# Kernel optimization log

Measured on AMD Instinct MI355X. Metric: run time of the kernel, lower is better.

The kernel has to match this reference:

```python
import jax, jax.numpy as jnp
import numpy as np


def setup_inputs() -> dict:
    key = jax.random.key(0)
    B, D = 1024, 65536
    inputs = jax.random.normal(key, (B, D), dtype=jnp.float32)
    return {"inputs": inputs, "k": 1024}


def reference(inputs, k):
    # top_k along last axis (matches tf.math.top_k)
    top_k_vals, _ = jax.lax.top_k(inputs, k)          # [B, k]
    # tf.math.reduce_min with no axis -> global scalar threshold
    threshold = jnp.min(top_k_vals)
    mask = jnp.where(inputs >= threshold, jnp.float32(1.0), jnp.float32(0.0))
    return mask * inputs
```

## Files before the change

### kernel.cpp

```cpp
#include <hip/hip_runtime.h>
#include <stdint.h>

#define TPB 256
#define NB1 2048
#define NB2 2048
#define NB3 1024
#define CAP 4096
#define DCOLS 65536

__device__ __forceinline__ unsigned f2key(float f) {
  unsigned u = __float_as_uint(f);
  unsigned m = ((int)u >> 31) | 0x80000000u;
  return u ^ m;
}
__device__ __forceinline__ float key2f(unsigned k) {
  unsigned u = (k & 0x80000000u) ? (k ^ 0x80000000u) : ~k;
  return __uint_as_float(u);
}

__device__ void find_top(const unsigned* hist, int NB, unsigned K,
                         unsigned* scan, unsigned* selbin, unsigned* selrem) {
  const int tid = threadIdx.x;
  const int C = NB / TPB;
  unsigned cs = 0;
  for (int i = 0; i < C; ++i) cs += hist[tid * C + i];
  scan[tid] = cs;
  __syncthreads();
  unsigned suff = cs;
  for (int off = 1; off < TPB; off <<= 1) {
    unsigned add = (tid + off < TPB) ? scan[tid + off] : 0u;
    __syncthreads();
    suff += add;
    scan[tid] = suff;
    __syncthreads();
  }
  unsigned above = suff - cs;
  if (above < K && suff >= K) {
    unsigned cAbove = above;
    for (int bin = tid * C + C - 1; bin >= tid * C; --bin) {
      unsigned c = hist[bin];
      if (cAbove + c >= K) { *selbin = (unsigned)bin; *selrem = K - cAbove; break; }
      cAbove += c;
    }
  }
  __syncthreads();
}

__global__ void __launch_bounds__(TPB)
topk_select(const float* __restrict__ in, const int* __restrict__ kptr,
            unsigned* __restrict__ rowkey) {
  __shared__ unsigned h1[NB1];
  __shared__ unsigned h2[NB2];
  __shared__ unsigned h3[NB3];
  __shared__ unsigned cand[CAP];
  __shared__ unsigned scan[TPB];
  __shared__ unsigned sel_bin, sel_rem, cand_cnt;

  const int tid = threadIdx.x;
  const int row = blockIdx.x;
  const unsigned K = (unsigned)(*kptr);

  for (int i = tid; i < NB1; i += TPB) h1[i] = 0u;
  for (int i = tid; i < NB2; i += TPB) h2[i] = 0u;
  for (int i = tid; i < NB3; i += TPB) h3[i] = 0u;
  if (tid == 0) cand_cnt = 0u;
  __syncthreads();

  const float4* rowv = (const float4*)(in + (size_t)row * DCOLS);
  const int n4 = DCOLS / 4;

  for (int i = tid; i < n4; i += TPB) {
    float4 v = rowv[i];
    atomicAdd(&h1[f2key(v.x) >> 21], 1u);
    atomicAdd(&h1[f2key(v.y) >> 21], 1u);
    atomicAdd(&h1[f2key(v.z) >> 21], 1u);
    atomicAdd(&h1[f2key(v.w) >> 21], 1u);
  }
  __syncthreads();
  find_top(h1, NB1, K, scan, &sel_bin, &sel_rem);
  const unsigned b1 = sel_bin;
  const unsigned K2 = sel_rem;
  __syncthreads();

  for (int i = tid; i < n4; i += TPB) {
    float4 v = rowv[i];
    unsigned kk;
    kk = f2key(v.x);
    if ((kk >> 21) == b1) { atomicAdd(&h2[(kk >> 10) & (NB2 - 1)], 1u);
      unsigned p = atomicAdd(&cand_cnt, 1u); if (p < CAP) cand[p] = kk; }
    kk = f2key(v.y);
    if ((kk >> 21) == b1) { atomicAdd(&h2[(kk >> 10) & (NB2 - 1)], 1u);
      unsigned p = atomicAdd(&cand_cnt, 1u); if (p < CAP) cand[p] = kk; }
    kk = f2key(v.z);
    if ((kk >> 21) == b1) { atomicAdd(&h2[(kk >> 10) & (NB2 - 1)], 1u);
      unsigned p = atomicAdd(&cand_cnt, 1u); if (p < CAP) cand[p] = kk; }
    kk = f2key(v.w);
    if ((kk >> 21) == b1) { atomicAdd(&h2[(kk >> 10) & (NB2 - 1)], 1u);
      unsigned p = atomicAdd(&cand_cnt, 1u); if (p < CAP) cand[p] = kk; }
  }
  __syncthreads();
  find_top(h2, NB2, K2, scan, &sel_bin, &sel_rem);
  const unsigned b2 = sel_bin;
  const unsigned K3 = sel_rem;
  const unsigned nc = cand_cnt;
  __syncthreads();

  if (nc <= CAP) {
    for (unsigned i = tid; i < nc; i += TPB) {
      unsigned kk = cand[i];
      if (((kk >> 10) & (NB2 - 1)) == b2) atomicAdd(&h3[kk & (NB3 - 1)], 1u);
    }
  } else {
    const unsigned pfx = (b1 << 11) | b2;
    for (int i = tid; i < n4; i += TPB) {
      float4 v = rowv[i];
      unsigned kk;
      kk = f2key(v.x); if ((kk >> 10) == pfx) atomicAdd(&h3[kk & (NB3 - 1)], 1u);
      kk = f2key(v.y); if ((kk >> 10) == pfx) atomicAdd(&h3[kk & (NB3 - 1)], 1u);
      kk = f2key(v.z); if ((kk >> 10) == pfx) atomicAdd(&h3[kk & (NB3 - 1)], 1u);
      kk = f2key(v.w); if ((kk >> 10) == pfx) atomicAdd(&h3[kk & (NB3 - 1)], 1u);
    }
  }
  __syncthreads();
  find_top(h3, NB3, K3, scan, &sel_bin, &sel_rem);
  if (tid == 0) rowkey[row] = (b1 << 21) | (b2 << 10) | sel_bin;
}

__global__ void __launch_bounds__(TPB)
minreduce(const unsigned* __restrict__ rowkey, unsigned* __restrict__ thr, int n) {
  __shared__ unsigned s[TPB];
  unsigned m = 0xFFFFFFFFu;
  for (int i = threadIdx.x; i < n; i += TPB) m = min(m, rowkey[i]);
  s[threadIdx.x] = m;
  __syncthreads();
  for (int off = TPB / 2; off > 0; off >>= 1) {
    if (threadIdx.x < off) s[threadIdx.x] = min(s[threadIdx.x], s[threadIdx.x + off]);
    __syncthreads();
  }
  if (threadIdx.x == 0) thr[0] = s[0];
}

__global__ void __launch_bounds__(TPB)
maskk(const float4* __restrict__ in, float4* __restrict__ out,
      const unsigned* __restrict__ thrkey, int n4) {
  const float thr = key2f(thrkey[0]);
  int idx = blockIdx.x * TPB + threadIdx.x;
  int stride = gridDim.x * TPB;
  for (int i = idx; i < n4; i += stride) {
    float4 v = in[i];
    float4 o;
    o.x = (v.x >= thr) ? v.x : 0.0f;
    o.y = (v.y >= thr) ? v.y : 0.0f;
    o.z = (v.z >= thr) ? v.z : 0.0f;
    o.w = (v.w >= thr) ? v.w : 0.0f;
    out[i] = o;
  }
}

extern "C" void kernel_launch(void* const* d_in, const int* in_sizes, int n_in,
                              void* d_out, int out_size, void* d_ws, size_t ws_size,
                              hipStream_t stream) {
  const float* in = (const float*)d_in[0];
  const int* kptr = (const int*)d_in[1];
  float* out = (float*)d_out;
  unsigned* rowkey = (unsigned*)d_ws;
  unsigned* thr = rowkey + 1024;

  const int B = in_sizes[0] / DCOLS;
  const int n4 = out_size / 4;

  hipLaunchKernelGGL(topk_select, dim3(B), dim3(TPB), 0, stream, in, kptr, rowkey);
  hipLaunchKernelGGL(minreduce, dim3(1), dim3(TPB), 0, stream, rowkey, thr, B);
  hipLaunchKernelGGL(maskk, dim3(2048), dim3(TPB), 0, stream,
                     (const float4*)in, (float4*)out, thr, n4);
}
```

Baseline: 538.6 us.

## Use sampled threshold to filter candidates and radix-select in shared memory

Builds a coarse histogram from the first 4096 elements of each row to estimate a conservative threshold near the k/8 sample rank. One full pass then compacts every element above that threshold into shared memory using wave ballot and one atomic per wave. All three radix-select levels run on that candidate list, which replaces two full-row passes with many per-element shared atomics. If the sample gives too few or too many candidates, it falls back to the original three full passes. The mask kernel grid is also doubled.

```diff
diff --git a/kernel.cpp b/kernel.cpp
--- a/kernel.cpp
+++ b/kernel.cpp
@@ -2,11 +2,11 @@
 #include <stdint.h>
 
 #define TPB 256
-#define NB1 2048
-#define NB2 2048
+#define NBH 2048
 #define NB3 1024
-#define CAP 4096
+#define CAP 6144
 #define DCOLS 65536
+#define NSAMP 4096
 
 __device__ __forceinline__ unsigned f2key(float f) {
   unsigned u = __float_as_uint(f);
@@ -16,6 +16,10 @@
 __device__ __forceinline__ float key2f(unsigned k) {
   unsigned u = (k & 0x80000000u) ? (k ^ 0x80000000u) : ~k;
   return __uint_as_float(u);
+}
+
+__device__ __forceinline__ void clear_hist(unsigned* hist, int NB) {
+  for (int i = threadIdx.x; i < NB; i += TPB) hist[i] = 0u;
 }
 
 __device__ void find_top(const unsigned* hist, int NB, unsigned K,
@@ -49,81 +53,129 @@
 __global__ void __launch_bounds__(TPB)
 topk_select(const float* __restrict__ in, const int* __restrict__ kptr,
             unsigned* __restrict__ rowkey) {
-  __shared__ unsigned h1[NB1];
-  __shared__ unsigned h2[NB2];
-  __shared__ unsigned h3[NB3];
+  __shared__ unsigned hist[NBH];
+  __shared__ unsigned scan[TPB];
   __shared__ unsigned cand[CAP];
-  __shared__ unsigned scan[TPB];
   __shared__ unsigned sel_bin, sel_rem, cand_cnt;
 
   const int tid = threadIdx.x;
+  const int lane = tid & 63;
   const int row = blockIdx.x;
   const unsigned K = (unsigned)(*kptr);
-
-  for (int i = tid; i < NB1; i += TPB) h1[i] = 0u;
-  for (int i = tid; i < NB2; i += TPB) h2[i] = 0u;
-  for (int i = tid; i < NB3; i += TPB) h3[i] = 0u;
-  if (tid == 0) cand_cnt = 0u;
-  __syncthreads();
-
   const float4* rowv = (const float4*)(in + (size_t)row * DCOLS);
   const int n4 = DCOLS / 4;
 
+  clear_hist(hist, NBH);
+  if (tid == 0) cand_cnt = 0u;
+  __syncthreads();
+  for (int j = 0; j < NSAMP / 4 / TPB; ++j) {
+    float4 v = rowv[tid + j * TPB];
+    atomicAdd(&hist[f2key(v.x) >> 21], 1u);
+    atomicAdd(&hist[f2key(v.y) >> 21], 1u);
+    atomicAdd(&hist[f2key(v.z) >> 21], 1u);
+    atomicAdd(&hist[f2key(v.w) >> 21], 1u);
+  }
+  __syncthreads();
+  unsigned ksamp = K >> 3;
+  if (ksamp < 32u) ksamp = 32u;
+  if (ksamp > NSAMP - 1) ksamp = NSAMP - 1;
+  find_top(hist, NBH, ksamp, scan, &sel_bin, &sel_rem);
+  const unsigned tlo = sel_bin << 21;
+  __syncthreads();
+
   for (int i = tid; i < n4; i += TPB) {
     float4 v = rowv[i];
-    atomicAdd(&h1[f2key(v.x) >> 21], 1u);
-    atomicAdd(&h1[f2key(v.y) >> 21], 1u);
-    atomicAdd(&h1[f2key(v.z) >> 21], 1u);
-    atomicAdd(&h1[f2key(v.w) >> 21], 1u);
-  }
-  __syncthreads();
-  find_top(h1, NB1, K, scan, &sel_bin, &sel_rem);
-  const unsigned b1 = sel_bin;
-  const unsigned K2 = sel_rem;
-  __syncthreads();
-
-  for (int i = tid; i < n4; i += TPB) {
-    float4 v = rowv[i];
-    unsigned kk;
-    kk = f2key(v.x);
-    if ((kk >> 21) == b1) { atomicAdd(&h2[(kk >> 10) & (NB2 - 1)], 1u);
-      unsigned p = atomicAdd(&cand_cnt, 1u); if (p < CAP) cand[p] = kk; }
-    kk = f2key(v.y);
-    if ((kk >> 21) == b1) { atomicAdd(&h2[(kk >> 10) & (NB2 - 1)], 1u);
-      unsigned p = atomicAdd(&cand_cnt, 1u); if (p < CAP) cand[p] = kk; }
-    kk = f2key(v.z);
-    if ((kk >> 21) == b1) { atomicAdd(&h2[(kk >> 10) & (NB2 - 1)], 1u);
-      unsigned p = atomicAdd(&cand_cnt, 1u); if (p < CAP) cand[p] = kk; }
-    kk = f2key(v.w);
-    if ((kk >> 21) == b1) { atomicAdd(&h2[(kk >> 10) & (NB2 - 1)], 1u);
-      unsigned p = atomicAdd(&cand_cnt, 1u); if (p < CAP) cand[p] = kk; }
-  }
-  __syncthreads();
-  find_top(h2, NB2, K2, scan, &sel_bin, &sel_rem);
-  const unsigned b2 = sel_bin;
-  const unsigned K3 = sel_rem;
+    unsigned kx = f2key(v.x), ky = f2key(v.y), kz = f2key(v.z), kw = f2key(v.w);
+#define CPCT(kk)                                                               \
+    {                                                                          \
+      bool p = (kk) >= tlo;                                                    \
+      unsigned long long m = __ballot(p);                                      \
+      if (m) {                                                                 \
+        unsigned base = 0;                                                     \
+        if (lane == 0) base = atomicAdd(&cand_cnt, (unsigned)__popcll(m));     \
+        base = __shfl(base, 0);                                                \
+        if (p) {                                                               \
+          unsigned off = base + (unsigned)__popcll(m & ((1ull << lane) - 1ull));\
+          if (off < CAP) cand[off] = (kk);                                     \
+        }                                                                      \
+      }                                                                        \
+    }
+    CPCT(kx) CPCT(ky) CPCT(kz) CPCT(kw)
+#undef CPCT
+  }
+  __syncthreads();
   const unsigned nc = cand_cnt;
   __syncthreads();
 
-  if (nc <= CAP) {
+  if (nc >= K && nc <= CAP) {
+    clear_hist(hist, NBH); __syncthreads();
+    for (unsigned i = tid; i < nc; i += TPB) atomicAdd(&hist[cand[i] >> 21], 1u);
+    __syncthreads();
+    find_top(hist, NBH, K, scan, &sel_bin, &sel_rem);
+    const unsigned b1 = sel_bin, K2 = sel_rem;
+    __syncthreads();
+
+    clear_hist(hist, NBH); __syncthreads();
     for (unsigned i = tid; i < nc; i += TPB) {
       unsigned kk = cand[i];
-      if (((kk >> 10) & (NB2 - 1)) == b2) atomicAdd(&h3[kk & (NB3 - 1)], 1u);
-    }
+      if ((kk >> 21) == b1) atomicAdd(&hist[(kk >> 10) & (NBH - 1)], 1u);
+    }
+    __syncthreads();
+    find_top(hist, NBH, K2, scan, &sel_bin, &sel_rem);
+    const unsigned b2 = sel_bin, K3 = sel_rem;
+    __syncthreads();
+
+    clear_hist(hist, NB3); __syncthreads();
+    const unsigned pfx = (b1 << 11) | b2;
+    for (unsigned i = tid; i < nc; i += TPB) {
+      unsigned kk = cand[i];
+      if ((kk >> 10) == pfx) atomicAdd(&hist[kk & (NB3 - 1)], 1u);
+    }
+    __syncthreads();
+    find_top(hist, NB3, K3, scan, &sel_bin, &sel_rem);
+    if (tid == 0) rowkey[row] = (b1 << 21) | (b2 << 10) | sel_bin;
   } else {
+    clear_hist(hist, NBH); __syncthreads();
+    for (int i = tid; i < n4; i += TPB) {
+      float4 v = rowv[i];
+      atomicAdd(&hist[f2key(v.x) >> 21], 1u);
+      atomicAdd(&hist[f2key(v.y) >> 21], 1u);
+      atomicAdd(&hist[f2key(v.z) >> 21], 1u);
+      atomicAdd(&hist[f2key(v.w) >> 21], 1u);
+    }
+    __syncthreads();
+    find_top(hist, NBH, K, scan, &sel_bin, &sel_rem);
+    const unsigned b1 = sel_bin, K2 = sel_rem;
+    __syncthreads();
+
+    clear_hist(hist, NBH); __syncthreads();
+    for (int i = tid; i < n4; i += TPB) {
+      float4 v = rowv[i];
+      unsigned kk;
+      kk = f2key(v.x); if ((kk >> 21) == b1) atomicAdd(&hist[(kk >> 10) & (NBH - 1)], 1u);
+      kk = f2key(v.y); if ((kk >> 21) == b1) atomicAdd(&hist[(kk >> 10) & (NBH - 1)], 1u);
+      kk = f2key(v.z); if ((kk >> 21) == b1) atomicAdd(&hist[(kk >> 10) & (NBH - 1)], 1u);
+      kk = f2key(v.w); if ((kk >> 21) == b1) atomicAdd(&hist[(kk >> 10) & (NBH - 1)], 1u);
+    }
+    __syncthreads();
+    find_top(hist, NBH, K2, scan, &sel_bin, &sel_rem);
+    const unsigned b2 = sel_bin, K3 = sel_rem;
+    __syncthreads();
+
+    clear_hist(hist, NB3); __syncthreads();
     const unsigned pfx = (b1 << 11) | b2;
     for (int i = tid; i < n4; i += TPB) {
       float4 v = rowv[i];
       unsigned kk;
-      kk = f2key(v.x); if ((kk >> 10) == pfx) atomicAdd(&h3[kk & (NB3 - 1)], 1u);
-      kk = f2key(v.y); if ((kk >> 10) == pfx) atomicAdd(&h3[kk & (NB3 - 1)], 1u);
-      kk = f2key(v.z); if ((kk >> 10) == pfx) atomicAdd(&h3[kk & (NB3 - 1)], 1u);
-      kk = f2key(v.w); if ((kk >> 10) == pfx) atomicAdd(&h3[kk & (NB3 - 1)], 1u);
-    }
-  }
-  __syncthreads();
-  find_top(h3, NB3, K3, scan, &sel_bin, &sel_rem);
-  if (tid == 0) rowkey[row] = (b1 << 21) | (b2 << 10) | sel_bin;
+      kk = f2key(v.x); if ((kk >> 10) == pfx) atomicAdd(&hist[kk & (NB3 - 1)], 1u);
+      kk = f2key(v.y); if ((kk >> 10) == pfx) atomicAdd(&hist[kk & (NB3 - 1)], 1u);
+      kk = f2key(v.z); if ((kk >> 10) == pfx) atomicAdd(&hist[kk & (NB3 - 1)], 1u);
+      kk = f2key(v.w); if ((kk >> 10) == pfx) atomicAdd(&hist[kk & (NB3 - 1)], 1u);
+    }
+    __syncthreads();
+    find_top(hist, NB3, K3, scan, &sel_bin, &sel_rem);
+    if (tid == 0) rowkey[row] = (b1 << 21) | (b2 << 10) | sel_bin;
+  }
 }
 
 __global__ void __launch_bounds__(TPB)
@@ -171,6 +223,6 @@
 
   hipLaunchKernelGGL(topk_select, dim3(B), dim3(TPB), 0, stream, in, kptr, rowkey);
   hipLaunchKernelGGL(minreduce, dim3(1), dim3(TPB), 0, stream, rowkey, thr, B);
-  hipLaunchKernelGGL(maskk, dim3(2048), dim3(TPB), 0, stream,
+  hipLaunchKernelGGL(maskk, dim3(4096), dim3(TPB), 0, stream,
                      (const float4*)in, (float4*)out, thr, n4);
 }
```

Result: faster. 512.3 us (-4.9%).
